# Kernel tuning notes

Hardware: AMD Instinct MI355X
Metric: run time of the kernel (lower is better)

## Reference

```python
import jax, jax.numpy as jnp
import numpy as np

N_NODES = 50000
N_EDGES = 800000
DIM_IN, DIM_H, DIM_OUT = 128, 128, 64


def _init_linear(key, fan_in, fan_out):
    # kaiming-uniform-ish init, matches torch Linear scale
    lim = 1.0 / np.sqrt(fan_in)
    return jax.random.uniform(key, (fan_in, fan_out), jnp.float32, -lim, lim)


def setup_inputs() -> dict:
    key = jax.random.key(0)
    ks = jax.random.split(key, 12)
    x = jax.random.normal(ks[0], (N_NODES, DIM_IN), jnp.float32)
    edge_index = jax.random.randint(ks[1], (2, N_EDGES), 0, N_NODES, jnp.int32)
    dims = [(DIM_IN, DIM_H), (DIM_H, DIM_H), (DIM_H, DIM_OUT)]
    inp = {"x": x, "edge_index": edge_index}
    for i, (fi, fo) in enumerate(dims):
        inp[f"Wl{i}"] = _init_linear(ks[2 + 3 * i], fi, fo)   # neighbor transform
        inp[f"Wr{i}"] = _init_linear(ks[3 + 3 * i], fi, fo)   # root transform
        inp[f"b{i}"] = jnp.zeros((fo,), jnp.float32)
    return inp


def _sage_layer(x, src, dst, Wl, Wr, b):
    # mean aggregation of neighbor messages x[src] at destination nodes
    msg = x[src]                                              # [E, d]
    agg = jax.ops.segment_sum(msg, dst, num_segments=N_NODES)  # [N, d]
    cnt = jax.ops.segment_sum(jnp.ones((src.shape[0],), x.dtype), dst,
                              num_segments=N_NODES)
    mean = agg / jnp.maximum(cnt, 1.0)[:, None]               # isolated nodes -> 0
    return mean @ Wl + b + x @ Wr                              # SAGEConv


def reference(x, edge_index, Wl0, Wr0, b0, Wl1, Wr1, b1, Wl2, Wr2, b2):
    src, dst = edge_index[0], edge_index[1]
    layers = [(Wl0, Wr0, b0), (Wl1, Wr1, b1), (Wl2, Wr2, b2)]
    h = x
    for i, (Wl, Wr, b) in enumerate(layers):
        h = _sage_layer(h, src, dst, Wl, Wr, b)
        if i != len(layers) - 1:
            h = jax.nn.relu(h)  # dropout p=0.2 is identity in eval mode
    return jax.nn.log_softmax(h, axis=1), h
```

## Files before the change

### kernel.cpp

```cpp
#include <hip/hip_runtime.h>

#define N_NODES 50000
#define N_EDGES 800000
#define SCAN_BLOCKS 196
#define WIN 6250

typedef __attribute__((ext_vector_type(8))) short short8;
typedef __attribute__((ext_vector_type(4))) float f32x4;
typedef unsigned short ushort_t;
typedef unsigned int uint_t;

__device__ inline ushort_t f2bf(float f) {
    union { float f; uint_t u; } v; v.f = f;
    uint_t u = v.u;
    u += 0x7fffu + ((u >> 16) & 1u);
    return (ushort_t)(u >> 16);
}
__device__ inline float bflo(uint_t v) { return __uint_as_float(v << 16); }
__device__ inline float bfhi(uint_t v) { return __uint_as_float(v & 0xffff0000u); }
__device__ inline float bf2f(ushort_t v) { return __uint_as_float((uint_t)v << 16); }

__global__ void count_edges_mp(const int* __restrict__ ei, int* __restrict__ cnt) {
    int g = blockIdx.x & 7;
    int nb = gridDim.x >> 3;
    int bi = blockIdx.x >> 3;
    int lo = g * WIN;
    for (int e = bi * 256 + threadIdx.x; e < N_EDGES; e += nb * 256) {
        int d = ei[N_EDGES + e];
        if ((unsigned)(d - lo) < WIN) atomicAdd(&cnt[d], 1);
    }
}

__global__ void fill_csr_mp(const int* __restrict__ ei, int* __restrict__ cursor,
                            int* __restrict__ csr_src) {
    int g = blockIdx.x & 7;
    int nb = gridDim.x >> 3;
    int bi = blockIdx.x >> 3;
    int lo = g * WIN;
    for (int e = bi * 256 + threadIdx.x; e < N_EDGES; e += nb * 256) {
        int d = ei[N_EDGES + e];
        if ((unsigned)(d - lo) < WIN) {
            int p = atomicAdd(&cursor[d], 1);
            csr_src[p] = ei[e];
        }
    }
}

__global__ void block_sums(const int* __restrict__ cnt, int* __restrict__ bsum) {
    int i = blockIdx.x * 256 + threadIdx.x;
    int v = (i < N_NODES) ? cnt[i] : 0;
    for (int off = 32; off; off >>= 1) v += __shfl_down(v, off, 64);
    __shared__ int s[4];
    if ((threadIdx.x & 63) == 0) s[threadIdx.x >> 6] = v;
    __syncthreads();
    if (threadIdx.x == 0) bsum[blockIdx.x] = s[0] + s[1] + s[2] + s[3];
}

__global__ void scan_bsums(const int* __restrict__ bsum, int* __restrict__ bprefix,
                           int* __restrict__ rowstart) {
    __shared__ int s[256];
    int t = threadIdx.x;
    int v = (t < SCAN_BLOCKS) ? bsum[t] : 0;
    s[t] = v;
    __syncthreads();
    for (int off = 1; off < 256; off <<= 1) {
        int add = (t >= off) ? s[t - off] : 0;
        __syncthreads();
        s[t] += add;
        __syncthreads();
    }
    bprefix[t] = s[t] - v;
    if (t == 0) rowstart[N_NODES] = N_EDGES;
}

__global__ void apply_scan(const int* __restrict__ cnt, const int* __restrict__ bprefix,
                           int* __restrict__ rowstart, int* __restrict__ cursor) {
    __shared__ int s[256];
    int t = threadIdx.x;
    int i = blockIdx.x * 256 + t;
    int v = (i < N_NODES) ? cnt[i] : 0;
    s[t] = v;
    __syncthreads();
    for (int off = 1; off < 256; off <<= 1) {
        int add = (t >= off) ? s[t - off] : 0;
        __syncthreads();
        s[t] += add;
        __syncthreads();
    }
    int excl = s[t] - v + bprefix[blockIdx.x];
    if (i < N_NODES) { rowstart[i] = excl; cursor[i] = excl; }
}

__global__ void cvt_bf16(const float* __restrict__ in, ushort_t* __restrict__ out, int n4) {
    int i = blockIdx.x * 256 + threadIdx.x;
    if (i < n4) {
        float4 v = ((const float4*)in)[i];
        ushort4 o;
        o.x = f2bf(v.x); o.y = f2bf(v.y); o.z = f2bf(v.z); o.w = f2bf(v.w);
        ((ushort4*)out)[i] = o;
    }
}

__global__ void pack_w256(const float* __restrict__ Wl, const float* __restrict__ Wr,
                          ushort_t* __restrict__ out) {
    int idx = blockIdx.x * 256 + threadIdx.x;
    if (idx >= 8 * 8 * 64 * 8) return;
    int j = idx & 7, l = (idx >> 3) & 63, t = (idx >> 9) & 7, ks = idx >> 12;
    int n = t * 16 + (l & 15);
    int k = ks * 32 + (l >> 4) * 8 + j;
    float w = (k < 128) ? Wl[k * 128 + n] : Wr[(k - 128) * 128 + n];
    out[idx] = f2bf(w);
}

__global__ void pack_wzr(const float* __restrict__ Wl, const float* __restrict__ Wr,
                         ushort_t* __restrict__ out) {
    int idx = blockIdx.x * 256 + threadIdx.x;
    if (idx >= 4 * 8 * 64 * 8) return;
    int j = idx & 7, l = (idx >> 3) & 63, t = (idx >> 9) & 7, ks = idx >> 12;
    int n = t * 16 + (l & 15);
    int k = ks * 32 + (l >> 4) * 8 + j;
    float w = (n < 64) ? Wl[k * 64 + n] : Wr[k * 64 + (n - 64)];
    out[idx] = f2bf(w);
}

__global__ void aggregate_bf(const ushort_t* __restrict__ hbf,
                             const int* __restrict__ rowstart,
                             const int* __restrict__ csr_src,
                             ushort_t* __restrict__ meanbf) {
    int node = blockIdx.x * 4 + (threadIdx.x >> 6);
    int lane = threadIdx.x & 63;
    if (node >= N_NODES) return;
    int s0 = rowstart[node], s1 = rowstart[node + 1];
    float ax = 0.f, ay = 0.f;
    const uint_t* base = (const uint_t*)hbf;
    for (int b = s0; b < s1; b += 64) {
        int m = min(64, s1 - b);
        int idx = (lane < m) ? csr_src[b + lane] : 0;
        int j = 0;
        for (; j + 8 <= m; j += 8) {
            uint_t v0 = base[(size_t)__shfl(idx, j + 0, 64) * 64 + lane];
            uint_t v1 = base[(size_t)__shfl(idx, j + 1, 64) * 64 + lane];
            uint_t v2 = base[(size_t)__shfl(idx, j + 2, 64) * 64 + lane];
            uint_t v3 = base[(size_t)__shfl(idx, j + 3, 64) * 64 + lane];
            uint_t v4 = base[(size_t)__shfl(idx, j + 4, 64) * 64 + lane];
            uint_t v5 = base[(size_t)__shfl(idx, j + 5, 64) * 64 + lane];
            uint_t v6 = base[(size_t)__shfl(idx, j + 6, 64) * 64 + lane];
            uint_t v7 = base[(size_t)__shfl(idx, j + 7, 64) * 64 + lane];
            ax += ((bflo(v0) + bflo(v1)) + (bflo(v2) + bflo(v3)))
                + ((bflo(v4) + bflo(v5)) + (bflo(v6) + bflo(v7)));
            ay += ((bfhi(v0) + bfhi(v1)) + (bfhi(v2) + bfhi(v3)))
                + ((bfhi(v4) + bfhi(v5)) + (bfhi(v6) + bfhi(v7)));
        }
        for (; j < m; ++j) {
            uint_t v = base[(size_t)__shfl(idx, j, 64) * 64 + lane];
            ax += bflo(v);
            ay += bfhi(v);
        }
    }
    float inv = 1.0f / fmaxf((float)(s1 - s0), 1.0f);
    ax *= inv; ay *= inv;
    uint_t packed = (uint_t)f2bf(ax) | ((uint_t)f2bf(ay) << 16);
    ((uint_t*)meanbf)[(size_t)node * 64 + lane] = packed;
}

__global__ __launch_bounds__(256) void sage_gemm_pk(
    const ushort_t* __restrict__ mean_bf, const ushort_t* __restrict__ root_bf,
    const ushort_t* __restrict__ Bpk, const float* __restrict__ bias,
    ushort_t* __restrict__ out_bf) {
    int lane = threadIdx.x & 63;
    int wave = threadIdx.x >> 6;
    int row16 = lane & 15;
    int quad = lane >> 4;
    int rowBase = blockIdx.x * 64 + wave * 16;
    int arow = min(rowBase + row16, N_NODES - 1);
    const ushort_t* mrow = mean_bf + (size_t)arow * 128;
    const ushort_t* rrow = root_bf + (size_t)arow * 128;
    const short8* bp = (const short8*)Bpk + lane;

    f32x4 acc[8];
    #pragma unroll
    for (int t = 0; t < 8; ++t) { f32x4 z = {0.f, 0.f, 0.f, 0.f}; acc[t] = z; }

    #pragma unroll
    for (int ks = 0; ks < 8; ++ks) {
        const ushort_t* src = (ks < 4) ? (mrow + ks * 32 + quad * 8)
                                       : (rrow + (ks - 4) * 32 + quad * 8);
        short8 afrag = *(const short8*)src;
        #pragma unroll
        for (int t = 0; t < 8; ++t) {
            short8 bfrag = bp[(ks * 8 + t) * 64];
            acc[t] = __builtin_amdgcn_mfma_f32_16x16x32_bf16(afrag, bfrag, acc[t], 0, 0, 0);
        }
    }

    #pragma unroll
    for (int t = 0; t < 8; ++t) {
        int col = t * 16 + row16;
        float bv = bias[col];
        #pragma unroll
        for (int r = 0; r < 4; ++r) {
            int row = rowBase + quad * 4 + r;
            if (row < N_NODES) {
                float v = fmaxf(acc[t][r] + bv, 0.f);
                out_bf[(size_t)row * 128 + col] = f2bf(v);
            }
        }
    }
}

__global__ __launch_bounds__(256) void gemm_zr_pk(
    const ushort_t* __restrict__ h_bf, const ushort_t* __restrict__ Bpk,
    const float* __restrict__ bias,
    ushort_t* __restrict__ z_bf, float* __restrict__ r_f32) {
    int lane = threadIdx.x & 63;
    int wave = threadIdx.x >> 6;
    int row16 = lane & 15;
    int quad = lane >> 4;
    int rowBase = blockIdx.x * 64 + wave * 16;
    int arow = min(rowBase + row16, N_NODES - 1);
    const ushort_t* hrow = h_bf + (size_t)arow * 128;
    const short8* bp = (const short8*)Bpk + lane;

    f32x4 acc[8];
    #pragma unroll
    for (int t = 0; t < 8; ++t) { f32x4 z = {0.f, 0.f, 0.f, 0.f}; acc[t] = z; }

    #pragma unroll
    for (int ks = 0; ks < 4; ++ks) {
        short8 afrag = *(const short8*)(hrow + ks * 32 + quad * 8);
        #pragma unroll
        for (int t = 0; t < 8; ++t) {
            short8 bfrag = bp[(ks * 8 + t) * 64];
            acc[t] = __builtin_amdgcn_mfma_f32_16x16x32_bf16(afrag, bfrag, acc[t], 0, 0, 0);
        }
    }

    #pragma unroll
    for (int t = 0; t < 8; ++t) {
        int col = t * 16 + row16;
        #pragma unroll
        for (int r = 0; r < 4; ++r) {
            int row = rowBase + quad * 4 + r;
            if (row < N_NODES) {
                if (col < 64) {
                    z_bf[(size_t)row * 64 + col] = f2bf(acc[t][r]);
                } else {
                    r_f32[(size_t)row * 64 + (col - 64)] = acc[t][r] + bias[col - 64];
                }
            }
        }
    }
}

__global__ void final_agg_softmax(const ushort_t* __restrict__ z_bf,
                                  const float* __restrict__ r_f32,
                                  const int* __restrict__ rowstart,
                                  const int* __restrict__ csr_src,
                                  float* __restrict__ out) {
    int node = blockIdx.x * 4 + (threadIdx.x >> 6);
    int lane = threadIdx.x & 63;
    if (node >= N_NODES) return;
    int s0 = rowstart[node], s1 = rowstart[node + 1];
    float a = 0.f;
    for (int b = s0; b < s1; b += 64) {
        int m = min(64, s1 - b);
        int idx = (lane < m) ? csr_src[b + lane] : 0;
        int j = 0;
        for (; j + 8 <= m; j += 8) {
            float v0 = bf2f(z_bf[(size_t)__shfl(idx, j + 0, 64) * 64 + lane]);
            float v1 = bf2f(z_bf[(size_t)__shfl(idx, j + 1, 64) * 64 + lane]);
            float v2 = bf2f(z_bf[(size_t)__shfl(idx, j + 2, 64) * 64 + lane]);
            float v3 = bf2f(z_bf[(size_t)__shfl(idx, j + 3, 64) * 64 + lane]);
            float v4 = bf2f(z_bf[(size_t)__shfl(idx, j + 4, 64) * 64 + lane]);
            float v5 = bf2f(z_bf[(size_t)__shfl(idx, j + 5, 64) * 64 + lane]);
            float v6 = bf2f(z_bf[(size_t)__shfl(idx, j + 6, 64) * 64 + lane]);
            float v7 = bf2f(z_bf[(size_t)__shfl(idx, j + 7, 64) * 64 + lane]);
            a += ((v0 + v1) + (v2 + v3)) + ((v4 + v5) + (v6 + v7));
        }
        for (; j < m; ++j)
            a += bf2f(z_bf[(size_t)__shfl(idx, j, 64) * 64 + lane]);
    }
    float inv = 1.0f / fmaxf((float)(s1 - s0), 1.0f);
    float h = a * inv + r_f32[(size_t)node * 64 + lane];
    float mx = h;
    for (int off = 32; off; off >>= 1) mx = fmaxf(mx, __shfl_xor(mx, off, 64));
    float e = expf(h - mx);
    float s = e;
    for (int off = 32; off; off >>= 1) s += __shfl_xor(s, off, 64);
    float lse = mx + logf(s);
    out[(size_t)node * 64 + lane] = h - lse;
    out[(size_t)N_NODES * 64 + (size_t)node * 64 + lane] = h;
}

extern "C" void kernel_launch(void* const* d_in, const int* in_sizes, int n_in,
                              void* d_out, int out_size, void* d_ws, size_t ws_size,
                              hipStream_t stream) {
    const float* x  = (const float*)d_in[0];
    const int* ei   = (const int*)d_in[1];
    const float* Wl0 = (const float*)d_in[2];
    const float* Wr0 = (const float*)d_in[3];
    const float* b0  = (const float*)d_in[4];
    const float* Wl1 = (const float*)d_in[5];
    const float* Wr1 = (const float*)d_in[6];
    const float* b1  = (const float*)d_in[7];
    const float* Wl2 = (const float*)d_in[8];
    const float* Wr2 = (const float*)d_in[9];
    const float* b2  = (const float*)d_in[10];
    float* out = (float*)d_out;

    char* ws = (char*)d_ws;
    int* cnt      = (int*)(ws + 0x000000);
    int* rowstart = (int*)(ws + 0x040000);
    int* cursor   = (int*)(ws + 0x080000);
    int* bsum     = (int*)(ws + 0x0C0000);
    int* bprefix  = (int*)(ws + 0x0C1000);
    int* csr_src  = (int*)(ws + 0x100000);
    ushort_t* pk0 = (ushort_t*)(ws + 0x420000);
    ushort_t* pk1 = (ushort_t*)(ws + 0x440000);
    ushort_t* pkz = (ushort_t*)(ws + 0x460000);
    ushort_t* x_bf    = (ushort_t*)(ws + 0x0500000);
    ushort_t* mean_bf = (ushort_t*)(ws + 0x1200000);
    ushort_t* h_bf    = (ushort_t*)(ws + 0x1F00000);
    ushort_t* z_bf    = (ushort_t*)(ws + 0x1200000);
    float*    r_f32   = (float*)  (ws + 0x0500000);

    pack_w256<<<128, 256, 0, stream>>>(Wl0, Wr0, pk0);
    pack_w256<<<128, 256, 0, stream>>>(Wl1, Wr1, pk1);
    pack_wzr<<<64, 256, 0, stream>>>(Wl2, Wr2, pkz);

    hipMemsetAsync(cnt, 0, N_NODES * sizeof(int), stream);
    count_edges_mp<<<1024, 256, 0, stream>>>(ei, cnt);
    block_sums<<<SCAN_BLOCKS, 256, 0, stream>>>(cnt, bsum);
    scan_bsums<<<1, 256, 0, stream>>>(bsum, bprefix, rowstart);
    apply_scan<<<SCAN_BLOCKS, 256, 0, stream>>>(cnt, bprefix, rowstart, cursor);
    fill_csr_mp<<<1024, 256, 0, stream>>>(ei, cursor, csr_src);

    cvt_bf16<<<6250, 256, 0, stream>>>(x, x_bf, (N_NODES * 128) / 4);

    aggregate_bf<<<12500, 256, 0, stream>>>(x_bf, rowstart, csr_src, mean_bf);
    sage_gemm_pk<<<782, 256, 0, stream>>>(mean_bf, x_bf, pk0, b0, h_bf);

    aggregate_bf<<<12500, 256, 0, stream>>>(h_bf, rowstart, csr_src, mean_bf);
    sage_gemm_pk<<<782, 256, 0, stream>>>(mean_bf, h_bf, pk1, b1, h_bf);

    gemm_zr_pk<<<782, 256, 0, stream>>>(h_bf, pkz, b2, z_bf, r_f32);
    final_agg_softmax<<<12500, 256, 0, stream>>>(z_bf, r_f32, rowstart, csr_src, out);
}
```

Before: 330.7 us.

## Fuse neighbor aggregation into SAGE GEMM kernels and merge prep kernels

Merges bf16 conversion, weight packing and count zeroing into one prep launch. Moves the per-node mean gather into the layer GEMM kernels, staging the mean tile in shared memory instead of writing it to global memory. Also fuses layer 1's GEMM with the layer 2 Z/R projection via LDS so h2 never goes to global. The cost is far fewer waves doing the gather (each wave serially handles 16 nodes), which reduces latency hiding for the random reads.

```diff
diff --git a/kernel.cpp b/kernel.cpp
--- a/kernel.cpp
+++ b/kernel.cpp
@@ -19,6 +19,43 @@
 __device__ inline float bflo(uint_t v) { return __uint_as_float(v << 16); }
 __device__ inline float bfhi(uint_t v) { return __uint_as_float(v & 0xffff0000u); }
 __device__ inline float bf2f(ushort_t v) { return __uint_as_float((uint_t)v << 16); }
+
+__global__ void prep(const float* __restrict__ x, uint_t* __restrict__ x_bf_u,
+                     const float* __restrict__ Wl0, const float* __restrict__ Wr0,
+                     const float* __restrict__ Wl1, const float* __restrict__ Wr1,
+                     const float* __restrict__ Wl2, const float* __restrict__ Wr2,
+                     ushort_t* __restrict__ pk0, ushort_t* __restrict__ pk1,
+                     ushort_t* __restrict__ pkz, int* __restrict__ cnt) {
+    int b = blockIdx.x, tid = threadIdx.x;
+    if (b < 6250) {
+        int i = b * 256 + tid;
+        float4 v = ((const float4*)x)[i];
+        uint_t lo = (uint_t)f2bf(v.x) | ((uint_t)f2bf(v.y) << 16);
+        uint_t hi = (uint_t)f2bf(v.z) | ((uint_t)f2bf(v.w) << 16);
+        x_bf_u[i * 2] = lo; x_bf_u[i * 2 + 1] = hi;
+    } else if (b < 6506) {
+        int bb = b - 6250;
+        const float* Wl = (bb < 128) ? Wl0 : Wl1;
+        const float* Wr = (bb < 128) ? Wr0 : Wr1;
+        ushort_t* out = (bb < 128) ? pk0 : pk1;
+        int idx = (bb & 127) * 256 + tid;
+        int j = idx & 7, l = (idx >> 3) & 63, t = (idx >> 9) & 7, ks = idx >> 12;
+        int n = t * 16 + (l & 15);
+        int k = ks * 32 + (l >> 4) * 8 + j;
+        float w = (k < 128) ? Wl[k * 128 + n] : Wr[(k - 128) * 128 + n];
+        out[idx] = f2bf(w);
+    } else if (b < 6570) {
+        int idx = (b - 6506) * 256 + tid;
+        int j = idx & 7, l = (idx >> 3) & 63, t = (idx >> 9) & 7, ks = idx >> 12;
+        int n = t * 16 + (l & 15);
+        int k = ks * 32 + (l >> 4) * 8 + j;
+        float w = (n < 64) ? Wl2[k * 64 + n] : Wr2[k * 64 + (n - 64)];
+        pkz[idx] = f2bf(w);
+    } else {
+        int i = (b - 6570) * 256 + tid;
+        if (i < 12500) ((int4*)cnt)[i] = make_int4(0, 0, 0, 0);
+    }
+}
 
 __global__ void count_edges_mp(const int* __restrict__ ei, int* __restrict__ cnt) {
     int g = blockIdx.x & 7;
@@ -91,48 +128,12 @@
     if (i < N_NODES) { rowstart[i] = excl; cursor[i] = excl; }
 }
 
-__global__ void cvt_bf16(const float* __restrict__ in, ushort_t* __restrict__ out, int n4) {
-    int i = blockIdx.x * 256 + threadIdx.x;
-    if (i < n4) {
-        float4 v = ((const float4*)in)[i];
-        ushort4 o;
-        o.x = f2bf(v.x); o.y = f2bf(v.y); o.z = f2bf(v.z); o.w = f2bf(v.w);
-        ((ushort4*)out)[i] = o;
-    }
-}
-
-__global__ void pack_w256(const float* __restrict__ Wl, const float* __restrict__ Wr,
-                          ushort_t* __restrict__ out) {
-    int idx = blockIdx.x * 256 + threadIdx.x;
-    if (idx >= 8 * 8 * 64 * 8) return;
-    int j = idx & 7, l = (idx >> 3) & 63, t = (idx >> 9) & 7, ks = idx >> 12;
-    int n = t * 16 + (l & 15);
-    int k = ks * 32 + (l >> 4) * 8 + j;
-    float w = (k < 128) ? Wl[k * 128 + n] : Wr[(k - 128) * 128 + n];
-    out[idx] = f2bf(w);
-}
-
-__global__ void pack_wzr(const float* __restrict__ Wl, const float* __restrict__ Wr,
-                         ushort_t* __restrict__ out) {
-    int idx = blockIdx.x * 256 + threadIdx.x;
-    if (idx >= 4 * 8 * 64 * 8) return;
-    int j = idx & 7, l = (idx >> 3) & 63, t = (idx >> 9) & 7, ks = idx >> 12;
-    int n = t * 16 + (l & 15);
-    int k = ks * 32 + (l >> 4) * 8 + j;
-    float w = (n < 64) ? Wl[k * 64 + n] : Wr[k * 64 + (n - 64)];
-    out[idx] = f2bf(w);
-}
-
-__global__ void aggregate_bf(const ushort_t* __restrict__ hbf,
-                             const int* __restrict__ rowstart,
-                             const int* __restrict__ csr_src,
-                             ushort_t* __restrict__ meanbf) {
-    int node = blockIdx.x * 4 + (threadIdx.x >> 6);
-    int lane = threadIdx.x & 63;
-    if (node >= N_NODES) return;
+__device__ inline void gather_mean(const uint_t* __restrict__ base,
+                                   const int* __restrict__ rowstart,
+                                   const int* __restrict__ csr_src,
+                                   int node, int lane, float& ax, float& ay) {
     int s0 = rowstart[node], s1 = rowstart[node + 1];
-    float ax = 0.f, ay = 0.f;
-    const uint_t* base = (const uint_t*)hbf;
+    ax = 0.f; ay = 0.f;
     for (int b = s0; b < s1; b += 64) {
         int m = min(64, s1 - b);
         int idx = (lane < m) ? csr_src[b + lane] : 0;
@@ -159,23 +160,30 @@
     }
     float inv = 1.0f / fmaxf((float)(s1 - s0), 1.0f);
     ax *= inv; ay *= inv;
-    uint_t packed = (uint_t)f2bf(ax) | ((uint_t)f2bf(ay) << 16);
-    ((uint_t*)meanbf)[(size_t)node * 64 + lane] = packed;
-}
-
-__global__ __launch_bounds__(256) void sage_gemm_pk(
-    const ushort_t* __restrict__ mean_bf, const ushort_t* __restrict__ root_bf,
+}
+
+__global__ __launch_bounds__(256) void layer0_fused(
+    const uint_t* __restrict__ xg, const ushort_t* __restrict__ x_root,
+    const int* __restrict__ rowstart, const int* __restrict__ csr_src,
     const ushort_t* __restrict__ Bpk, const float* __restrict__ bias,
-    ushort_t* __restrict__ out_bf) {
-    int lane = threadIdx.x & 63;
-    int wave = threadIdx.x >> 6;
-    int row16 = lane & 15;
-    int quad = lane >> 4;
-    int rowBase = blockIdx.x * 64 + wave * 16;
-    int arow = min(rowBase + row16, N_NODES - 1);
-    const ushort_t* mrow = mean_bf + (size_t)arow * 128;
-    const ushort_t* rrow = root_bf + (size_t)arow * 128;
+    ushort_t* __restrict__ h1) {
+    __shared__ ushort_t Ash[4][16 * 136];
+    int lane = threadIdx.x & 63, wave = threadIdx.x >> 6;
+    ushort_t* my = Ash[wave];
+    int nodeBase = blockIdx.x * 64 + wave * 16;
+
+    for (int m = 0; m < 16; ++m) {
+        int node = nodeBase + m;
+        float ax = 0.f, ay = 0.f;
+        if (node < N_NODES) gather_mean(xg, rowstart, csr_src, node, lane, ax, ay);
+        uint_t packed = (uint_t)f2bf(ax) | ((uint_t)f2bf(ay) << 16);
+        ((uint_t*)(my + m * 136))[lane] = packed;
+    }
+
+    int row16 = lane & 15, quad = lane >> 4;
     const short8* bp = (const short8*)Bpk + lane;
+    int rootRow = min(nodeBase + row16, N_NODES - 1);
+    const ushort_t* rrow = x_root + (size_t)rootRow * 128;
 
     f32x4 acc[8];
     #pragma unroll
@@ -183,9 +191,9 @@
 
     #pragma unroll
     for (int ks = 0; ks < 8; ++ks) {
-        const ushort_t* src = (ks < 4) ? (mrow + ks * 32 + quad * 8)
-                                       : (rrow + (ks - 4) * 32 + quad * 8);
-        short8 afrag = *(const short8*)src;
+        short8 afrag;
+        if (ks < 4) afrag = *(const short8*)&my[row16 * 136 + ks * 32 + quad * 8];
+        else        afrag = *(const short8*)(rrow + (ks - 4) * 32 + quad * 8);
         #pragma unroll
         for (int t = 0; t < 8; ++t) {
             short8 bfrag = bp[(ks * 8 + t) * 64];
@@ -199,35 +207,48 @@
         float bv = bias[col];
         #pragma unroll
         for (int r = 0; r < 4; ++r) {
-            int row = rowBase + quad * 4 + r;
+            int row = nodeBase + quad * 4 + r;
             if (row < N_NODES) {
                 float v = fmaxf(acc[t][r] + bv, 0.f);
-                out_bf[(size_t)row * 128 + col] = f2bf(v);
+                h1[(size_t)row * 128 + col] = f2bf(v);
             }
         }
     }
 }
 
-__global__ __launch_bounds__(256) void gemm_zr_pk(
-    const ushort_t* __restrict__ h_bf, const ushort_t* __restrict__ Bpk,
-    const float* __restrict__ bias,
+__global__ __launch_bounds__(256) void layer12_fused(
+    const uint_t* __restrict__ h1g, const ushort_t* __restrict__ h1_root,
+    const int* __restrict__ rowstart, const int* __restrict__ csr_src,
+    const ushort_t* __restrict__ Bpk1, const float* __restrict__ bias1,
+    const ushort_t* __restrict__ Bpkz, const float* __restrict__ bias2,
     ushort_t* __restrict__ z_bf, float* __restrict__ r_f32) {
-    int lane = threadIdx.x & 63;
-    int wave = threadIdx.x >> 6;
-    int row16 = lane & 15;
-    int quad = lane >> 4;
-    int rowBase = blockIdx.x * 64 + wave * 16;
-    int arow = min(rowBase + row16, N_NODES - 1);
-    const ushort_t* hrow = h_bf + (size_t)arow * 128;
-    const short8* bp = (const short8*)Bpk + lane;
+    __shared__ ushort_t Ash[4][16 * 136];
+    int lane = threadIdx.x & 63, wave = threadIdx.x >> 6;
+    ushort_t* my = Ash[wave];
+    int nodeBase = blockIdx.x * 64 + wave * 16;
+
+    for (int m = 0; m < 16; ++m) {
+        int node = nodeBase + m;
+        float ax = 0.f, ay = 0.f;
+        if (node < N_NODES) gather_mean(h1g, rowstart, csr_src, node, lane, ax, ay);
+        uint_t packed = (uint_t)f2bf(ax) | ((uint_t)f2bf(ay) << 16);
+        ((uint_t*)(my + m * 136))[lane] = packed;
+    }
+
+    int row16 = lane & 15, quad = lane >> 4;
+    const short8* bp = (const short8*)Bpk1 + lane;
+    int rootRow = min(nodeBase + row16, N_NODES - 1);
+    const ushort_t* rrow = h1_root + (size_t)rootRow * 128;
 
     f32x4 acc[8];
     #pragma unroll
     for (int t = 0; t < 8; ++t) { f32x4 z = {0.f, 0.f, 0.f, 0.f}; acc[t] = z; }
 
     #pragma unroll
-    for (int ks = 0; ks < 4; ++ks) {
-        short8 afrag = *(const short8*)(hrow + ks * 32 + quad * 8);
+    for (int ks = 0; ks < 8; ++ks) {
+        short8 afrag;
+        if (ks < 4) afrag = *(const short8*)&my[row16 * 136 + ks * 32 + quad * 8];
+        else        afrag = *(const short8*)(rrow + (ks - 4) * 32 + quad * 8);
         #pragma unroll
         for (int t = 0; t < 8; ++t) {
             short8 bfrag = bp[(ks * 8 + t) * 64];
@@ -238,15 +259,38 @@
     #pragma unroll
     for (int t = 0; t < 8; ++t) {
         int col = t * 16 + row16;
+        float bv = bias1[col];
         #pragma unroll
         for (int r = 0; r < 4; ++r) {
-            int row = rowBase + quad * 4 + r;
+            float v = fmaxf(acc[t][r] + bv, 0.f);
+            my[(quad * 4 + r) * 136 + col] = f2bf(v);
+        }
+    }
+
+    const short8* bpz = (const short8*)Bpkz + lane;
+    f32x4 accz[8];
+    #pragma unroll
+    for (int t = 0; t < 8; ++t) { f32x4 z = {0.f, 0.f, 0.f, 0.f}; accz[t] = z; }
+
+    #pragma unroll
+    for (int ks = 0; ks < 4; ++ks) {
+        short8 afrag = *(const short8*)&my[row16 * 136 + ks * 32 + quad * 8];
+        #pragma unroll
+        for (int t = 0; t < 8; ++t) {
+            short8 bfrag = bpz[(ks * 8 + t) * 64];
+            accz[t] = __builtin_amdgcn_mfma_f32_16x16x32_bf16(afrag, bfrag, accz[t], 0, 0, 0);
+        }
+    }
+
+    #pragma unroll
+    for (int t = 0; t < 8; ++t) {
+        int col = t * 16 + row16;
+        #pragma unroll
+        for (int r = 0; r < 4; ++r) {
+            int row = nodeBase + quad * 4 + r;
             if (row < N_NODES) {
-                if (col < 64) {
-                    z_bf[(size_t)row * 64 + col] = f2bf(acc[t][r]);
-                } else {
-                    r_f32[(size_t)row * 64 + (col - 64)] = acc[t][r] + bias[col - 64];
-                }
+                if (col < 64) z_bf[(size_t)row * 64 + col] = f2bf(accz[t][r]);
+                else          r_f32[(size_t)row * 64 + (col - 64)] = accz[t][r] + bias2[col - 64];
             }
         }
     }
@@ -318,31 +362,25 @@
     ushort_t* pk0 = (ushort_t*)(ws + 0x420000);
     ushort_t* pk1 = (ushort_t*)(ws + 0x440000);
     ushort_t* pkz = (ushort_t*)(ws + 0x460000);
-    ushort_t* x_bf    = (ushort_t*)(ws + 0x0500000);
-    ushort_t* mean_bf = (ushort_t*)(ws + 0x1200000);
-    ushort_t* h_bf    = (ushort_t*)(ws + 0x1F00000);
-    ushort_t* z_bf    = (ushort_t*)(ws + 0x1200000);
-    float*    r_f32   = (float*)  (ws + 0x0500000);
-
-    pack_w256<<<128, 256, 0, stream>>>(Wl0, Wr0, pk0);
-    pack_w256<<<128, 256, 0, stream>>>(Wl1, Wr1, pk1);
-    pack_wzr<<<64, 256, 0, stream>>>(Wl2, Wr2, pkz);
-
-    hipMemsetAsync(cnt, 0, N_NODES * sizeof(int), stream);
+    ushort_t* x_bf = (ushort_t*)(ws + 0x0500000);
+    ushort_t* h1   = (ushort_t*)(ws + 0x1F00000);
+    ushort_t* z_bf = (ushort_t*)(ws + 0x1200000);
+    float*    r_f32 = (float*)  (ws + 0x0500000);
+
+    prep<<<6619, 256, 0, stream>>>(x, (uint_t*)x_bf, Wl0, Wr0, Wl1, Wr1, Wl2, Wr2,
+                                   pk0, pk1, pkz, cnt);
+
     count_edges_mp<<<1024, 256, 0, stream>>>(ei, cnt);
     block_sums<<<SCAN_BLOCKS, 256, 0, stream>>>(cnt, bsum);
     scan_bsums<<<1, 256, 0, stream>>>(bsum, bprefix, rowstart);
     apply_scan<<<SCAN_BLOCKS, 256, 0, stream>>>(cnt, bprefix, rowstart, cursor);
     fill_csr_mp<<<1024, 256, 0, stream>>>(ei, cursor, csr_src);
 
-    cvt_bf16<<<6250, 256, 0, stream>>>(x, x_bf, (N_NODES * 128) / 4);
-
-    aggregate_bf<<<12500, 256, 0, stream>>>(x_bf, rowstart, csr_src, mean_bf);
-    sage_gemm_pk<<<782, 256, 0, stream>>>(mean_bf, x_bf, pk0, b0, h_bf);
-
-    aggregate_bf<<<12500, 256, 0, stream>>>(h_bf, rowstart, csr_src, mean_bf);
-    sage_gemm_pk<<<782, 256, 0, stream>>>(mean_bf, h_bf, pk1, b1, h_bf);
-
-    gemm_zr_pk<<<782, 256, 0, stream>>>(h_bf, pkz, b2, z_bf, r_f32);
+    layer0_fused<<<782, 256, 0, stream>>>((const uint_t*)x_bf, x_bf, rowstart, csr_src,
+                                          pk0, b0, h1);
+
+    layer12_fused<<<782, 256, 0, stream>>>((const uint_t*)h1, h1, rowstart, csr_src,
+                                           pk1, b1, pkz, b2, z_bf, r_f32);
+
     final_agg_softmax<<<12500, 256, 0, stream>>>(z_bf, r_f32, rowstart, csr_src, out);
 }
```

Measured after the change: 375.1 us. 1.13x slower.
